# Kernel optimization log

Measured on AMD Instinct MI355X. Metric: run time of the kernel, lower is better.

The kernel has to match this reference:

```python
import jax, jax.numpy as jnp
import numpy as np

N = 100000   # nodes
E = 1600000  # edges (avg degree 16)
D = 128      # input_dim = embedding_dim = output_dim
NEG_SLOPE = 0.01  # nn.LeakyReLU default


def setup_inputs() -> dict:
    key = jax.random.key(0)
    k0, k1, k2, k3, k4, k5 = jax.random.split(key, 6)
    x = jax.random.normal(k0, (N, D), jnp.float32)
    edge_index = jax.random.randint(k1, (2, E), 0, N, dtype=jnp.int32)
    batch = jnp.zeros((N,), jnp.int32)
    # GCNConv params (glorot-ish scale)
    W1 = jax.random.normal(k2, (D, D), jnp.float32) * 0.05
    b1 = jax.random.normal(k3, (D,), jnp.float32) * 0.05
    W2 = jax.random.normal(k4, (D, D), jnp.float32) * 0.05
    b2 = jax.random.normal(k5, (D,), jnp.float32) * 0.05
    return {"x": x, "W1": W1, "b1": b1, "W2": W2, "b2": b2,
            "edge_index": edge_index, "batch": batch}


def _gcn_conv(x, W, b, src, dst, deg_isqrt):
    # x' = D^{-1/2} (A + I) D^{-1/2} (x W) + b   (PyG GCNConv defaults)
    h = x @ W                                   # [N, D]
    coef = deg_isqrt[src] * deg_isqrt[dst]      # [E]
    msg = h[src] * coef[:, None]                # [E, D] gather + scale
    out = jax.ops.segment_sum(msg, dst, num_segments=N)  # scatter-add
    out = out + h * (deg_isqrt * deg_isqrt)[:, None]      # self-loop term
    return out + b


def reference(x, W1, b1, W2, b2, edge_index, batch):
    src, dst = edge_index[0], edge_index[1]
    # degree on A + I (self loops), same for both layers
    deg = jax.ops.segment_sum(jnp.ones((E,), x.dtype), dst, num_segments=N) + 1.0
    deg_isqrt = jax.lax.rsqrt(deg)
    h = _gcn_conv(x, W1, b1, src, dst, deg_isqrt)
    h = jax.nn.leaky_relu(h, NEG_SLOPE)
    h = _gcn_conv(h, W2, b2, src, dst, deg_isqrt)
    return jax.nn.leaky_relu(h, NEG_SLOPE)
```

## Files before the change

kernel.cpp:

```cpp
#include <hip/hip_runtime.h>
#include <hip/hip_bf16.h>
#include <stdint.h>

#define NN 100000
#define NE 1600000
#define NR (NE + NN)
#define DD 128
#define NEG 0.01f
#define NB 391
#define CAPSH 13
#define NBLKE 391
#define NWB 65

typedef __attribute__((ext_vector_type(8))) short short8;
typedef __attribute__((ext_vector_type(4))) float floatx4;
typedef __attribute__((ext_vector_type(4))) uint32_t uint32x4;

__device__ __forceinline__ uint16_t f2bf(float f){
  uint32_t i = __float_as_uint(f);
  return (uint16_t)((i + 0x7FFFu + ((i >> 16) & 1u)) >> 16);
}
__device__ __forceinline__ float lrelu(float x){ return fmaxf(x, NEG * x); }

__global__ __launch_bounds__(512) void k_init(const uint32_t* __restrict__ xw,
                                              int* __restrict__ flag,
                                              int* __restrict__ gcur){
  int t = threadIdx.x;
  if (t < NB) gcur[t] = 0;
  if (t < 64){
    uint32_t w = xw[t];
    uint32_t e = (w >> 7) & 0xFFu;
    int plaus = (e >= 100u && e <= 134u) ? 1 : 0;
    unsigned long long b = __ballot(plaus);
    if (t == 0) flag[0] = (__popcll(b) >= 48) ? 0 : 1;
  }
}

__global__ __launch_bounds__(512) void k_scat1(const int* __restrict__ src,
                                               const int* __restrict__ dst,
                                               int* __restrict__ gcur,
                                               uint64_t* __restrict__ pairs,
                                               const void* __restrict__ W1,
                                               const void* __restrict__ W2,
                                               const void* __restrict__ b1,
                                               const void* __restrict__ b2,
                                               uint16_t* __restrict__ WT1,
                                               uint16_t* __restrict__ WT2,
                                               uint16_t* __restrict__ bb,
                                               const int* __restrict__ flag){
  int t = threadIdx.x, b = blockIdx.x;
  if (b >= NBLKE){
    int j = (b - NBLKE) * 512 + t;
    int f = flag[0];
    if (j < 16384){
      int c = j >> 7, k = j & 127;
      WT1[j] = f ? f2bf(((const float*)W1)[k * DD + c])
                 : ((const uint16_t*)W1)[k * DD + c];
    } else if (j < 32768){
      int q = j - 16384;
      int c = q >> 7, k = q & 127;
      WT2[q] = f ? f2bf(((const float*)W2)[k * DD + c])
                 : ((const uint16_t*)W2)[k * DD + c];
    } else if (j < 33024){
      int q = j - 32768;
      const void* sp = (q < 128) ? b1 : b2;
      int i2 = q & 127;
      bb[q] = f ? f2bf(((const float*)sp)[i2]) : ((const uint16_t*)sp)[i2];
    }
    return;
  }
  __shared__ int lh[NB];
  if (t < NB) lh[t] = 0;
  __syncthreads();
  int ds[8], ss[8];
  #pragma unroll
  for (int i = 0; i < 8; i++){
    int e = b * 4096 + i * 512 + t;
    if (e < NE){
      ds[i] = dst[e]; ss[i] = src[e];
      atomicAdd(&lh[ds[i] >> 8], 1);
    } else ds[i] = -1;
  }
  __syncthreads();
  if (t < NB){
    int c = lh[t];
    int base = c ? atomicAdd(&gcur[t], c) : 0;
    lh[t] = (t << CAPSH) + base;
  }
  __syncthreads();
  #pragma unroll
  for (int i = 0; i < 8; i++){
    if (ds[i] >= 0){
      int bkt = ds[i] >> 8;
      int pos = atomicAdd(&lh[bkt], 1);
      if (pos < ((bkt + 1) << CAPSH))
        pairs[pos] = ((uint64_t)(uint32_t)ds[i] << 32) | (uint32_t)ss[i];
    }
  }
}

__global__ __launch_bounds__(512) void k_bsort_a(const uint64_t* __restrict__ pairs,
                                                 const int* __restrict__ gcur,
                                                 int2* __restrict__ pairs2,
                                                 int* __restrict__ prow,
                                                 float* __restrict__ dis){
  __shared__ int sg[512];
  __shared__ int lcnt[256], sm[256];
  __shared__ int s_pe;
  int t = threadIdx.x, bkt = blockIdx.x, n0 = bkt << 8;
  int v0 = (t < NB) ? gcur[t] : 0;
  sg[t] = v0;
  __syncthreads();
  for (int s = 1; s < 512; s <<= 1){
    int add = (t >= s) ? sg[t - s] : 0;
    __syncthreads();
    sg[t] += add;
    __syncthreads();
  }
  if (t == bkt) s_pe = sg[t] - v0;
  if (t < 256) lcnt[t] = 0;
  __syncthreads();
  int cnt = gcur[bkt];
  int begE = bkt << CAPSH;
  for (int i = t; i < cnt; i += 512)
    atomicAdd(&lcnt[(int)(pairs[begE + i] >> 32) - n0], 1);
  __syncthreads();
  int inb = (n0 + t < NN) ? 1 : 0;
  int v = (t < 256) ? lcnt[t] + inb : 0;
  if (t < 256) sm[t] = v;
  __syncthreads();
  for (int s = 1; s < 256; s <<= 1){
    int add = (t < 256 && t >= s) ? sm[t - s] : 0;
    __syncthreads();
    if (t < 256) sm[t] += add;
    __syncthreads();
  }
  if (t < 256){
    int n = n0 + t;
    int begS = s_pe + n0;
    int excl = sm[t] - v;
    if (n <= NN) prow[n] = begS + excl;
    if (n < NN){
      float dn = rsqrtf((float)(lcnt[t] + 1));
      dis[n] = dn;
      pairs2[begS + excl] = make_int2(n, __float_as_int(dn * dn));
    }
  }
}

__global__ __launch_bounds__(512) void k_bsort_b(const uint64_t* __restrict__ pairs,
                                                 const int* __restrict__ gcur,
                                                 const int* __restrict__ prow,
                                                 const float* __restrict__ dis,
                                                 int2* __restrict__ pairs2){
  __shared__ int cur[256];
  __shared__ float ddn[256];
  int t = threadIdx.x, bkt = blockIdx.x, n0 = bkt << 8;
  if (t < 256){
    int n = n0 + t;
    cur[t] = (n < NN) ? prow[n] + 1 : 0;
    ddn[t] = (n < NN) ? dis[n] : 0.f;
  }
  __syncthreads();
  int cnt = gcur[bkt];
  int begE = bkt << CAPSH;
  for (int i = t; i < cnt; i += 512){
    uint64_t u = pairs[begE + i];
    int d = (int)(u >> 32), s = (int)(uint32_t)u;
    int li = d - n0;
    int pos = atomicAdd(&cur[li], 1);
    pairs2[pos] = make_int2(s, __float_as_int(ddn[li] * dis[s]));
  }
}

__device__ __forceinline__ short8 ldcvt(const float* __restrict__ p){
  floatx4 u = ((const floatx4*)p)[0], v = ((const floatx4*)p)[1];
  short8 r;
  r[0] = (short)f2bf(u.x); r[1] = (short)f2bf(u.y);
  r[2] = (short)f2bf(u.z); r[3] = (short)f2bf(u.w);
  r[4] = (short)f2bf(v.x); r[5] = (short)f2bf(v.y);
  r[6] = (short)f2bf(v.z); r[7] = (short)f2bf(v.w);
  return r;
}

__global__ __launch_bounds__(256) void k_gemm(const void* __restrict__ X,
                                              const uint16_t* __restrict__ WT,
                                              uint16_t* __restrict__ H,
                                              const int* __restrict__ flag,
                                              int xf32){
  __shared__ uint16_t lwt[128 * 136];
  int t = threadIdx.x;
  const uint32_t* wt32 = (const uint32_t*)WT;
  #pragma unroll
  for (int i = 0; i < 32; i++){
    int uidx = t + 256 * i;
    uint32_t w2 = wt32[uidx];
    int el = uidx * 2;
    int c = el >> 7, k = el & 127;
    *(uint32_t*)&lwt[c * 136 + k] = w2;
  }
  __syncthreads();

  int wave = t >> 6, lane = t & 63;
  int m = lane & 15, q = lane >> 4;
  int rowbase = blockIdx.x * 64 + wave * 16;
  int ar = rowbase + m;
  if (ar >= NN) ar = 0;
  short8 a0, a1, a2, a3;
  if (xf32 && flag[0]){
    const float* xr = (const float*)X + (size_t)ar * DD;
    a0 = ldcvt(xr + q * 8);        a1 = ldcvt(xr + (q + 4) * 8);
    a2 = ldcvt(xr + (q + 8) * 8);  a3 = ldcvt(xr + (q + 12) * 8);
  } else {
    const short8* xrow = (const short8*)((const uint16_t*)X + (size_t)ar * DD);
    a0 = xrow[q]; a1 = xrow[q + 4]; a2 = xrow[q + 8]; a3 = xrow[q + 12];
  }

  #pragma unroll
  for (int nt = 0; nt < 8; nt++){
    int c = nt * 16 + m;
    const uint16_t* bp = &lwt[c * 136 + q * 8];
    floatx4 acc = {0.f, 0.f, 0.f, 0.f};
    acc = __builtin_amdgcn_mfma_f32_16x16x32_bf16(a0, *(const short8*)(bp +  0), acc, 0, 0, 0);
    acc = __builtin_amdgcn_mfma_f32_16x16x32_bf16(a1, *(const short8*)(bp + 32), acc, 0, 0, 0);
    acc = __builtin_amdgcn_mfma_f32_16x16x32_bf16(a2, *(const short8*)(bp + 64), acc, 0, 0, 0);
    acc = __builtin_amdgcn_mfma_f32_16x16x32_bf16(a3, *(const short8*)(bp + 96), acc, 0, 0, 0);
    #pragma unroll
    for (int r = 0; r < 4; r++){
      int row = rowbase + q * 4 + r;
      if (row < NN) H[(size_t)row * DD + c] = f2bf(acc[r]);
    }
  }
}

#define FMA8(VA, CF)                                                     \
  acc[0] = fmaf(__uint_as_float(VA.x << 16),         CF, acc[0]);        \
  acc[1] = fmaf(__uint_as_float(VA.x & 0xffff0000u), CF, acc[1]);        \
  acc[2] = fmaf(__uint_as_float(VA.y << 16),         CF, acc[2]);        \
  acc[3] = fmaf(__uint_as_float(VA.y & 0xffff0000u), CF, acc[3]);        \
  acc[4] = fmaf(__uint_as_float(VA.z << 16),         CF, acc[4]);        \
  acc[5] = fmaf(__uint_as_float(VA.z & 0xffff0000u), CF, acc[5]);        \
  acc[6] = fmaf(__uint_as_float(VA.w << 16),         CF, acc[6]);        \
  acc[7] = fmaf(__uint_as_float(VA.w & 0xffff0000u), CF, acc[7]);

__global__ __launch_bounds__(256) void k_agg(const uint16_t* __restrict__ H,
                                             const int* __restrict__ prow,
                                             const int2* __restrict__ pairs2,
                                             const uint16_t* __restrict__ bias,
                                             void* __restrict__ OUT,
                                             const int* __restrict__ flag,
                                             int is_final){
  __shared__ int2 ebuf[4][96];
  int wave = threadIdx.x >> 6, lane = threadIdx.x & 63;
  int grp = lane >> 4, sl = lane & 15;
  if (lane >= 32) ebuf[wave][32 + lane] = make_int2(0, 0);
  int n = blockIdx.x * 4 + wave;
  if (n >= NN) return;
  int beg = prow[n], end = prow[n + 1];

  float acc[8] = {0.f,0.f,0.f,0.f,0.f,0.f,0.f,0.f};
  for (int j0 = beg; j0 < end; j0 += 64){
    int cnt = min(64, end - j0);
    int2 r = (lane < cnt) ? pairs2[j0 + lane] : make_int2(0, 0);
    ebuf[wave][lane] = r;
    int chunks = (cnt + 3) >> 2;
    int2 e0 = ebuf[wave][grp];
    int2 e1 = ebuf[wave][4 + grp];
    int2 e2 = ebuf[wave][8 + grp];
    uint32x4 v0 = *(const uint32x4*)(H + (size_t)e0.x * DD + sl * 8);
    uint32x4 v1 = *(const uint32x4*)(H + (size_t)e1.x * DD + sl * 8);
    uint32x4 v2 = *(const uint32x4*)(H + (size_t)e2.x * DD + sl * 8);
    for (int c = 0; c < chunks; c += 3){
      int2 n0 = ebuf[wave][(c + 3) * 4 + grp];
      int2 n1 = ebuf[wave][(c + 4) * 4 + grp];
      int2 n2 = ebuf[wave][(c + 5) * 4 + grp];
      uint32x4 w0 = *(const uint32x4*)(H + (size_t)n0.x * DD + sl * 8);
      uint32x4 w1 = *(const uint32x4*)(H + (size_t)n1.x * DD + sl * 8);
      uint32x4 w2 = *(const uint32x4*)(H + (size_t)n2.x * DD + sl * 8);
      float c0 = __int_as_float(e0.y);
      FMA8(v0, c0)
      float c1 = __int_as_float(e1.y);
      FMA8(v1, c1)
      float c2 = __int_as_float(e2.y);
      FMA8(v2, c2)
      e0 = n0; e1 = n1; e2 = n2;
      v0 = w0; v1 = w1; v2 = w2;
    }
  }
  #pragma unroll
  for (int j = 0; j < 8; j++){
    acc[j] += __shfl_xor(acc[j], 16, 64);
    acc[j] += __shfl_xor(acc[j], 32, 64);
  }
  uint32x4 bv = ((const uint32x4*)bias)[sl];
  float o0 = lrelu(acc[0] + __uint_as_float(bv.x << 16));
  float o1 = lrelu(acc[1] + __uint_as_float(bv.x & 0xffff0000u));
  float o2 = lrelu(acc[2] + __uint_as_float(bv.y << 16));
  float o3 = lrelu(acc[3] + __uint_as_float(bv.y & 0xffff0000u));
  float o4 = lrelu(acc[4] + __uint_as_float(bv.z << 16));
  float o5 = lrelu(acc[5] + __uint_as_float(bv.z & 0xffff0000u));
  float o6 = lrelu(acc[6] + __uint_as_float(bv.w << 16));
  float o7 = lrelu(acc[7] + __uint_as_float(bv.w & 0xffff0000u));
  if (is_final && flag[0]){
    float* orow = (float*)OUT + (size_t)n * DD + sl * 8;
    if (lane < 16){ floatx4 vv = {o0, o1, o2, o3}; ((floatx4*)orow)[0] = vv; }
    else if (lane < 32){ floatx4 vv = {o4, o5, o6, o7}; ((floatx4*)orow)[1] = vv; }
  } else if (lane < 16){
    uint32x4 pv;
    pv.x = (uint32_t)f2bf(o0) | ((uint32_t)f2bf(o1) << 16);
    pv.y = (uint32_t)f2bf(o2) | ((uint32_t)f2bf(o3) << 16);
    pv.z = (uint32_t)f2bf(o4) | ((uint32_t)f2bf(o5) << 16);
    pv.w = (uint32_t)f2bf(o6) | ((uint32_t)f2bf(o7) << 16);
    *(uint32x4*)((uint16_t*)OUT + (size_t)n * DD + sl * 8) = pv;
  }
}

extern "C" void kernel_launch(void* const* d_in, const int* in_sizes, int n_in,
                              void* d_out, int out_size, void* d_ws, size_t ws_size,
                              hipStream_t stream){
  const void* x  = d_in[0];
  const void* W1 = d_in[1];
  const void* b1 = d_in[2];
  const void* W2 = d_in[3];
  const void* b2 = d_in[4];
  const int* ei   = (const int*)d_in[5];
  const int* esrc = ei;
  const int* edst = ei + NE;

  char* ws = (char*)d_ws;
  float*    dis        = (float*)(ws + 0);
  int*      prow       = (int*)(ws + 512ull * 1024);
  int*      flag       = (int*)(ws + 960ull * 1024);
  uint16_t* WT1        = (uint16_t*)(ws + 964ull * 1024);
  uint16_t* WT2        = (uint16_t*)(ws + 996ull * 1024);
  uint16_t* bb         = (uint16_t*)(ws + 1028ull * 1024);
  int*      gcur       = (int*)(ws + 1032ull * 1024);
  int2*     pairs2     = (int2*)(ws + 2048ull * 1024);
  uint64_t* pairs      = (uint64_t*)(ws + 16320ull * 1024);
  uint16_t* hA         = (uint16_t*)(ws + 16384ull * 1024);
  uint16_t* hB         = (uint16_t*)d_out;

  k_init   <<<1, 512, 0, stream>>>((const uint32_t*)x, flag, gcur);
  k_scat1  <<<NBLKE + NWB, 512, 0, stream>>>(esrc, edst, gcur, pairs,
                                             W1, W2, b1, b2, WT1, WT2, bb, flag);
  k_bsort_a<<<NB, 512, 0, stream>>>(pairs, gcur, pairs2, prow, dis);
  k_bsort_b<<<NB, 512, 0, stream>>>(pairs, gcur, prow, dis, pairs2);

  k_gemm<<<(NN + 63) / 64, 256, 0, stream>>>(x, WT1, hA, flag, 1);
  k_agg <<<NN / 4, 256, 0, stream>>>(hA, prow, pairs2, bb, hB, flag, 0);
  k_gemm<<<(NN + 63) / 64, 256, 0, stream>>>(hB, WT2, hA, flag, 0);
  k_agg <<<NN / 4, 256, 0, stream>>>(hA, prow, pairs2, bb + 128, d_out, flag, 1);
}
```

Measured before the change: 301.3 us.

## Merge first GEMM into bucket-sort kernels and drop init kernel

Splits the first-layer GEMM across extra blocks appended to the two bucket-sort kernels, so the GEMM runs concurrently with the CSR build instead of as a separate launch. Also folds dtype detection into the scatter kernel, replaces the init kernel with a memset, retiles the GEMM to 512 threads covering 256 rows with two row tiles per wave, and moves the temporary pairs buffer into the output buffer. This removes launches and idle tail time but adds LDS pressure from the shared union, and relies on the output buffer being free until the first aggregation.

```diff
diff --git a/kernel.cpp b/kernel.cpp
--- a/kernel.cpp
+++ b/kernel.cpp
@@ -11,6 +11,8 @@
 #define CAPSH 13
 #define NBLKE 391
 #define NWB 65
+#define NG1 196
+#define NG2 195
 
 typedef __attribute__((ext_vector_type(8))) short short8;
 typedef __attribute__((ext_vector_type(4))) float floatx4;
@@ -22,24 +24,18 @@
 }
 __device__ __forceinline__ float lrelu(float x){ return fmaxf(x, NEG * x); }
 
-__global__ __launch_bounds__(512) void k_init(const uint32_t* __restrict__ xw,
-                                              int* __restrict__ flag,
-                                              int* __restrict__ gcur){
-  int t = threadIdx.x;
-  if (t < NB) gcur[t] = 0;
-  if (t < 64){
-    uint32_t w = xw[t];
-    uint32_t e = (w >> 7) & 0xFFu;
-    int plaus = (e >= 100u && e <= 134u) ? 1 : 0;
-    unsigned long long b = __ballot(plaus);
-    if (t == 0) flag[0] = (__popcll(b) >= 48) ? 0 : 1;
-  }
+__device__ __forceinline__ int detect_f32(const uint32_t* __restrict__ xw){
+  uint32_t w = xw[threadIdx.x & 63];
+  uint32_t e = (w >> 7) & 0xFFu;
+  unsigned long long b = __ballot(e >= 100u && e <= 134u);
+  return (__popcll(b) >= 48) ? 0 : 1;
 }
 
 __global__ __launch_bounds__(512) void k_scat1(const int* __restrict__ src,
                                                const int* __restrict__ dst,
                                                int* __restrict__ gcur,
                                                uint64_t* __restrict__ pairs,
+                                               const uint32_t* __restrict__ xw,
                                                const void* __restrict__ W1,
                                                const void* __restrict__ W2,
                                                const void* __restrict__ b1,
@@ -47,11 +43,12 @@
                                                uint16_t* __restrict__ WT1,
                                                uint16_t* __restrict__ WT2,
                                                uint16_t* __restrict__ bb,
-                                               const int* __restrict__ flag){
+                                               int* __restrict__ flag){
   int t = threadIdx.x, b = blockIdx.x;
   if (b >= NBLKE){
+    int f = detect_f32(xw);
+    if (b == NBLKE && t == 0) flag[0] = f;
     int j = (b - NBLKE) * 512 + t;
-    int f = flag[0];
     if (j < 16384){
       int c = j >> 7, k = j & 127;
       WT1[j] = f ? f2bf(((const float*)W1)[k * DD + c])
@@ -99,80 +96,6 @@
   }
 }
 
-__global__ __launch_bounds__(512) void k_bsort_a(const uint64_t* __restrict__ pairs,
-                                                 const int* __restrict__ gcur,
-                                                 int2* __restrict__ pairs2,
-                                                 int* __restrict__ prow,
-                                                 float* __restrict__ dis){
-  __shared__ int sg[512];
-  __shared__ int lcnt[256], sm[256];
-  __shared__ int s_pe;
-  int t = threadIdx.x, bkt = blockIdx.x, n0 = bkt << 8;
-  int v0 = (t < NB) ? gcur[t] : 0;
-  sg[t] = v0;
-  __syncthreads();
-  for (int s = 1; s < 512; s <<= 1){
-    int add = (t >= s) ? sg[t - s] : 0;
-    __syncthreads();
-    sg[t] += add;
-    __syncthreads();
-  }
-  if (t == bkt) s_pe = sg[t] - v0;
-  if (t < 256) lcnt[t] = 0;
-  __syncthreads();
-  int cnt = gcur[bkt];
-  int begE = bkt << CAPSH;
-  for (int i = t; i < cnt; i += 512)
-    atomicAdd(&lcnt[(int)(pairs[begE + i] >> 32) - n0], 1);
-  __syncthreads();
-  int inb = (n0 + t < NN) ? 1 : 0;
-  int v = (t < 256) ? lcnt[t] + inb : 0;
-  if (t < 256) sm[t] = v;
-  __syncthreads();
-  for (int s = 1; s < 256; s <<= 1){
-    int add = (t < 256 && t >= s) ? sm[t - s] : 0;
-    __syncthreads();
-    if (t < 256) sm[t] += add;
-    __syncthreads();
-  }
-  if (t < 256){
-    int n = n0 + t;
-    int begS = s_pe + n0;
-    int excl = sm[t] - v;
-    if (n <= NN) prow[n] = begS + excl;
-    if (n < NN){
-      float dn = rsqrtf((float)(lcnt[t] + 1));
-      dis[n] = dn;
-      pairs2[begS + excl] = make_int2(n, __float_as_int(dn * dn));
-    }
-  }
-}
-
-__global__ __launch_bounds__(512) void k_bsort_b(const uint64_t* __restrict__ pairs,
-                                                 const int* __restrict__ gcur,
-                                                 const int* __restrict__ prow,
-                                                 const float* __restrict__ dis,
-                                                 int2* __restrict__ pairs2){
-  __shared__ int cur[256];
-  __shared__ float ddn[256];
-  int t = threadIdx.x, bkt = blockIdx.x, n0 = bkt << 8;
-  if (t < 256){
-    int n = n0 + t;
-    cur[t] = (n < NN) ? prow[n] + 1 : 0;
-    ddn[t] = (n < NN) ? dis[n] : 0.f;
-  }
-  __syncthreads();
-  int cnt = gcur[bkt];
-  int begE = bkt << CAPSH;
-  for (int i = t; i < cnt; i += 512){
-    uint64_t u = pairs[begE + i];
-    int d = (int)(u >> 32), s = (int)(uint32_t)u;
-    int li = d - n0;
-    int pos = atomicAdd(&cur[li], 1);
-    pairs2[pos] = make_int2(s, __float_as_int(ddn[li] * dis[s]));
-  }
-}
-
 __device__ __forceinline__ short8 ldcvt(const float* __restrict__ p){
   floatx4 u = ((const floatx4*)p)[0], v = ((const floatx4*)p)[1];
   short8 r;
@@ -183,54 +106,170 @@
   return r;
 }
 
-__global__ __launch_bounds__(256) void k_gemm(const void* __restrict__ X,
-                                              const uint16_t* __restrict__ WT,
-                                              uint16_t* __restrict__ H,
-                                              const int* __restrict__ flag,
-                                              int xf32){
-  __shared__ uint16_t lwt[128 * 136];
+__device__ __forceinline__ void gemm_block(const void* __restrict__ X,
+                                           const uint16_t* __restrict__ WT,
+                                           uint16_t* __restrict__ H,
+                                           int row0, int xf32,
+                                           uint16_t* lwt ){
   int t = threadIdx.x;
-  const uint32_t* wt32 = (const uint32_t*)WT;
-  #pragma unroll
-  for (int i = 0; i < 32; i++){
-    int uidx = t + 256 * i;
-    uint32_t w2 = wt32[uidx];
-    int el = uidx * 2;
-    int c = el >> 7, k = el & 127;
-    *(uint32_t*)&lwt[c * 136 + k] = w2;
-  }
-  __syncthreads();
-
   int wave = t >> 6, lane = t & 63;
   int m = lane & 15, q = lane >> 4;
-  int rowbase = blockIdx.x * 64 + wave * 16;
-  int ar = rowbase + m;
-  if (ar >= NN) ar = 0;
-  short8 a0, a1, a2, a3;
-  if (xf32 && flag[0]){
-    const float* xr = (const float*)X + (size_t)ar * DD;
-    a0 = ldcvt(xr + q * 8);        a1 = ldcvt(xr + (q + 4) * 8);
-    a2 = ldcvt(xr + (q + 8) * 8);  a3 = ldcvt(xr + (q + 12) * 8);
+  int rowbase = row0 + wave * 32;
+  int ar0 = rowbase + m, ar1 = rowbase + 16 + m;
+  if (ar0 >= NN) ar0 = 0;
+  if (ar1 >= NN) ar1 = 0;
+  short8 a00, a01, a02, a03, a10, a11, a12, a13;
+  if (xf32){
+    const float* x0 = (const float*)X + (size_t)ar0 * DD;
+    a00 = ldcvt(x0 + q * 8);        a01 = ldcvt(x0 + (q + 4) * 8);
+    a02 = ldcvt(x0 + (q + 8) * 8);  a03 = ldcvt(x0 + (q + 12) * 8);
+    const float* x1 = (const float*)X + (size_t)ar1 * DD;
+    a10 = ldcvt(x1 + q * 8);        a11 = ldcvt(x1 + (q + 4) * 8);
+    a12 = ldcvt(x1 + (q + 8) * 8);  a13 = ldcvt(x1 + (q + 12) * 8);
   } else {
-    const short8* xrow = (const short8*)((const uint16_t*)X + (size_t)ar * DD);
-    a0 = xrow[q]; a1 = xrow[q + 4]; a2 = xrow[q + 8]; a3 = xrow[q + 12];
-  }
-
+    const short8* x0 = (const short8*)((const uint16_t*)X + (size_t)ar0 * DD);
+    a00 = x0[q]; a01 = x0[q + 4]; a02 = x0[q + 8]; a03 = x0[q + 12];
+    const short8* x1 = (const short8*)((const uint16_t*)X + (size_t)ar1 * DD);
+    a10 = x1[q]; a11 = x1[q + 4]; a12 = x1[q + 8]; a13 = x1[q + 12];
+  }
+  const uint32_t* wt32 = (const uint32_t*)WT;
+  #pragma unroll
+  for (int i = 0; i < 16; i++){
+    int uidx = t + 512 * i;
+    uint32_t w2 = wt32[uidx];
+    int c = uidx >> 6, k = (uidx * 2) & 127;
+    *(uint32_t*)&lwt[c * 136 + k] = w2;
+  }
+  __syncthreads();
   #pragma unroll
   for (int nt = 0; nt < 8; nt++){
     int c = nt * 16 + m;
     const uint16_t* bp = &lwt[c * 136 + q * 8];
-    floatx4 acc = {0.f, 0.f, 0.f, 0.f};
-    acc = __builtin_amdgcn_mfma_f32_16x16x32_bf16(a0, *(const short8*)(bp +  0), acc, 0, 0, 0);
-    acc = __builtin_amdgcn_mfma_f32_16x16x32_bf16(a1, *(const short8*)(bp + 32), acc, 0, 0, 0);
-    acc = __builtin_amdgcn_mfma_f32_16x16x32_bf16(a2, *(const short8*)(bp + 64), acc, 0, 0, 0);
-    acc = __builtin_amdgcn_mfma_f32_16x16x32_bf16(a3, *(const short8*)(bp + 96), acc, 0, 0, 0);
+    short8 b0 = *(const short8*)(bp +  0);
+    short8 b1 = *(const short8*)(bp + 32);
+    short8 b2 = *(const short8*)(bp + 64);
+    short8 b3 = *(const short8*)(bp + 96);
+    floatx4 acc0 = {0.f, 0.f, 0.f, 0.f};
+    floatx4 acc1 = {0.f, 0.f, 0.f, 0.f};
+    acc0 = __builtin_amdgcn_mfma_f32_16x16x32_bf16(a00, b0, acc0, 0, 0, 0);
+    acc0 = __builtin_amdgcn_mfma_f32_16x16x32_bf16(a01, b1, acc0, 0, 0, 0);
+    acc0 = __builtin_amdgcn_mfma_f32_16x16x32_bf16(a02, b2, acc0, 0, 0, 0);
+    acc0 = __builtin_amdgcn_mfma_f32_16x16x32_bf16(a03, b3, acc0, 0, 0, 0);
+    acc1 = __builtin_amdgcn_mfma_f32_16x16x32_bf16(a10, b0, acc1, 0, 0, 0);
+    acc1 = __builtin_amdgcn_mfma_f32_16x16x32_bf16(a11, b1, acc1, 0, 0, 0);
+    acc1 = __builtin_amdgcn_mfma_f32_16x16x32_bf16(a12, b2, acc1, 0, 0, 0);
+    acc1 = __builtin_amdgcn_mfma_f32_16x16x32_bf16(a13, b3, acc1, 0, 0, 0);
     #pragma unroll
     for (int r = 0; r < 4; r++){
       int row = rowbase + q * 4 + r;
-      if (row < NN) H[(size_t)row * DD + c] = f2bf(acc[r]);
-    }
-  }
+      if (row < NN) H[(size_t)row * DD + c] = f2bf(acc0[r]);
+      int row1 = row + 16;
+      if (row1 < NN) H[(size_t)row1 * DD + c] = f2bf(acc1[r]);
+    }
+  }
+}
+
+__global__ __launch_bounds__(512) void k_m1(const uint64_t* __restrict__ pairs,
+                                            const int* __restrict__ gcur,
+                                            int2* __restrict__ pairs2,
+                                            int* __restrict__ prow,
+                                            float* __restrict__ dis,
+                                            const void* __restrict__ X,
+                                            const uint16_t* __restrict__ WT1,
+                                            uint16_t* __restrict__ H,
+                                            const int* __restrict__ flag){
+  __shared__ union ShmM1 {
+    uint16_t lwt[128 * 136];
+    struct { int sg[512]; int lcnt[256]; int sm[256]; int pe; } a;
+  } u;
+  int t = threadIdx.x, b = blockIdx.x;
+  if (b >= NB){
+    gemm_block(X, WT1, H, (b - NB) * 256, flag[0], u.lwt);
+    return;
+  }
+  int bkt = b, n0 = bkt << 8;
+  int v0 = (t < NB) ? gcur[t] : 0;
+  u.a.sg[t] = v0;
+  __syncthreads();
+  for (int s = 1; s < 512; s <<= 1){
+    int add = (t >= s) ? u.a.sg[t - s] : 0;
+    __syncthreads();
+    u.a.sg[t] += add;
+    __syncthreads();
+  }
+  if (t == bkt) u.a.pe = u.a.sg[t] - v0;
+  if (t < 256) u.a.lcnt[t] = 0;
+  __syncthreads();
+  int cnt = gcur[bkt];
+  int begE = bkt << CAPSH;
+  for (int i = t; i < cnt; i += 512)
+    atomicAdd(&u.a.lcnt[(int)(pairs[begE + i] >> 32) - n0], 1);
+  __syncthreads();
+  int inb = (n0 + t < NN) ? 1 : 0;
+  int v = (t < 256) ? u.a.lcnt[t] + inb : 0;
+  if (t < 256) u.a.sm[t] = v;
+  __syncthreads();
+  for (int s = 1; s < 256; s <<= 1){
+    int add = (t < 256 && t >= s) ? u.a.sm[t - s] : 0;
+    __syncthreads();
+    if (t < 256) u.a.sm[t] += add;
+    __syncthreads();
+  }
+  if (t < 256){
+    int n = n0 + t;
+    int begS = u.a.pe + n0;
+    int excl = u.a.sm[t] - v;
+    if (n <= NN) prow[n] = begS + excl;
+    if (n < NN){
+      float dn = rsqrtf((float)(u.a.lcnt[t] + 1));
+      dis[n] = dn;
+      pairs2[begS + excl] = make_int2(n, __float_as_int(dn * dn));
+    }
+  }
+}
+
+__global__ __launch_bounds__(512) void k_m2(const uint64_t* __restrict__ pairs,
+                                            const int* __restrict__ gcur,
+                                            const int* __restrict__ prow,
+                                            const float* __restrict__ dis,
+                                            int2* __restrict__ pairs2,
+                                            const void* __restrict__ X,
+                                            const uint16_t* __restrict__ WT1,
+                                            uint16_t* __restrict__ H,
+                                            const int* __restrict__ flag){
+  __shared__ union ShmM2 {
+    uint16_t lwt[128 * 136];
+    struct { int cur[256]; float ddn[256]; } bw;
+  } u;
+  int t = threadIdx.x, b = blockIdx.x;
+  if (b >= NB){
+    gemm_block(X, WT1, H, (NG1 + (b - NB)) * 256, flag[0], u.lwt);
+    return;
+  }
+  int bkt = b, n0 = bkt << 8;
+  if (t < 256){
+    int n = n0 + t;
+    u.bw.cur[t] = (n < NN) ? prow[n] + 1 : 0;
+    u.bw.ddn[t] = (n < NN) ? dis[n] : 0.f;
+  }
+  __syncthreads();
+  int cnt = gcur[bkt];
+  int begE = bkt << CAPSH;
+  for (int i = t; i < cnt; i += 512){
+    uint64_t uu = pairs[begE + i];
+    int d = (int)(uu >> 32), s = (int)(uint32_t)uu;
+    int li = d - n0;
+    int pos = atomicAdd(&u.bw.cur[li], 1);
+    pairs2[pos] = make_int2(s, __float_as_int(u.bw.ddn[li] * dis[s]));
+  }
+}
+
+__global__ __launch_bounds__(512) void k_gemm(const void* __restrict__ X,
+                                              const uint16_t* __restrict__ WT,
+                                              uint16_t* __restrict__ H,
+                                              int xf32){
+  __shared__ uint16_t lwt[128 * 136];
+  gemm_block(X, WT, H, blockIdx.x * 256, xf32, lwt);
 }
 
 #define FMA8(VA, CF)                                                     \
@@ -336,18 +375,19 @@
   uint16_t* bb         = (uint16_t*)(ws + 1028ull * 1024);
   int*      gcur       = (int*)(ws + 1032ull * 1024);
   int2*     pairs2     = (int2*)(ws + 2048ull * 1024);
-  uint64_t* pairs      = (uint64_t*)(ws + 16320ull * 1024);
   uint16_t* hA         = (uint16_t*)(ws + 16384ull * 1024);
+  uint64_t* pairs      = (uint64_t*)d_out;
   uint16_t* hB         = (uint16_t*)d_out;
 
-  k_init   <<<1, 512, 0, stream>>>((const uint32_t*)x, flag, gcur);
-  k_scat1  <<<NBLKE + NWB, 512, 0, stream>>>(esrc, edst, gcur, pairs,
-                                             W1, W2, b1, b2, WT1, WT2, bb, flag);
-  k_bsort_a<<<NB, 512, 0, stream>>>(pairs, gcur, pairs2, prow, dis);
-  k_bsort_b<<<NB, 512, 0, stream>>>(pairs, gcur, prow, dis, pairs2);
-
-  k_gemm<<<(NN + 63) / 64, 256, 0, stream>>>(x, WT1, hA, flag, 1);
+  hipMemsetAsync(gcur, 0, NB * sizeof(int), stream);
+  k_scat1<<<NBLKE + NWB, 512, 0, stream>>>(esrc, edst, gcur, pairs,
+                                           (const uint32_t*)x,
+                                           W1, W2, b1, b2, WT1, WT2, bb, flag);
+  k_m1 <<<NB + NG1, 512, 0, stream>>>(pairs, gcur, pairs2, prow, dis,
+                                      x, WT1, hA, flag);
+  k_m2 <<<NB + NG2, 512, 0, stream>>>(pairs, gcur, prow, dis, pairs2,
+                                      x, WT1, hA, flag);
   k_agg <<<NN / 4, 256, 0, stream>>>(hA, prow, pairs2, bb, hB, flag, 0);
-  k_gemm<<<(NN + 63) / 64, 256, 0, stream>>>(hB, WT2, hA, flag, 0);
+  k_gemm<<<391, 512, 0, stream>>>(hB, WT2, hA, 0);
   k_agg <<<NN / 4, 256, 0, stream>>>(hA, prow, pairs2, bb + 128, d_out, flag, 1);
 }
```

New measurement: 307.6 us. 2.1% more time.
